# Performance work log

Hardware: AMD Instinct MI355X
Metric: run time of the kernel (lower is better)

Reference implementation:

```python
import jax, jax.numpy as jnp
import numpy as np

NW, OBS, HS, HS2, HM, CTX, ACT = 2048, 512, 512, 512, 256, 128, 18


def setup_inputs() -> dict:
    key = jax.random.key(0)
    ks = jax.random.split(key, 20)
    s = 0.02  # small init so tanh/softmax/sigmoid stay in sane range
    f32 = jnp.float32
    return {
        "obs": jax.random.normal(ks[0], (NW, 1, OBS), f32),
        "hidden_memory": jax.random.normal(ks[1], (1, NW, HM), f32),
        # fnn: Linear(obs_size, hidden_size)
        "W1": (jax.random.normal(ks[2], (HS, OBS), f32) * s),
        "b1": jnp.zeros((HS,), f32),
        # context: Linear(hidden_memory_size + 1, context_size)
        "Wc": (jax.random.normal(ks[3], (CTX, HM + 1), f32) * s),
        "bc": jnp.zeros((CTX,), f32),
        # attention: Linear(context_size, 1)
        "Wa": (jax.random.normal(ks[4], (1, CTX), f32) * s),
        "ba": jnp.zeros((1,), f32),
        # GRU(input=1, hidden=HM)
        "W_ih": (jax.random.normal(ks[5], (3 * HM, 1), f32) * s),
        "b_ih": jnp.zeros((3 * HM,), f32),
        "W_hh": (jax.random.normal(ks[6], (3 * HM, HM), f32) * s),
        "b_hh": jnp.zeros((3 * HM,), f32),
        # fnn2: Linear(hidden_size + hidden_memory_size, hidden_size_2)
        "W2": (jax.random.normal(ks[7], (HS2, HS + HM), f32) * s),
        "b2": jnp.zeros((HS2,), f32),
        # actor / critic heads
        "Wact": (jax.random.normal(ks[8], (ACT, HS2), f32) * s),
        "bact": jnp.zeros((ACT,), f32),
        "Wcrit": (jax.random.normal(ks[9], (1, HS2), f32) * s),
        "bcrit": jnp.zeros((1,), f32),
    }


def reference(obs, hidden_memory, W1, b1, Wc, bc, Wa, ba,
              W_ih, b_ih, W_hh, b_hh, W2, b2, Wact, bact, Wcrit, bcrit):
    # obs: [NW, 1, OBS], hidden_memory: [1, NW, HM]
    feat = jax.nn.relu(jnp.einsum('bto,ho->bth', obs, W1) + b1)  # [NW,1,HS]

    # context: Linear([obs_scalar, hidden_memory]) + tanh.
    # Split the (HM+1)-dim contraction: col 0 multiplies the obs scalar,
    # cols 1: contract with the broadcast hidden memory (same math as the
    # torch cat + Linear, without materializing the [NW,1,OBS,HM+1] tensor).
    h = jnp.swapaxes(hidden_memory, 0, 1)                        # [NW,1,HM]
    h_term = jnp.einsum('btm,cm->btc', h, Wc[:, 1:]) + bc        # [NW,1,CTX]
    ctx = jnp.tanh(obs[..., None] * Wc[:, 0] + h_term[:, :, None, :])  # [NW,1,OBS,CTX]

    # attention: Linear(CTX -> 1) then softmax over the obs dimension (dim=-2
    # of [...,OBS,1] == OBS after squeeze)
    alog = jnp.einsum('btoc,c->bto', ctx, Wa[0]) + ba[0]         # [NW,1,OBS]
    attn = jax.nn.softmax(alog, axis=-1)
    dset = jnp.sum(attn * obs, axis=-1, keepdims=True)           # [NW,1,1]

    # single-step GRU (torch gate ordering: r, z, n)
    x = dset[:, 0, :]                                            # [NW,1]
    hp = hidden_memory[0]                                        # [NW,HM]
    gi = x @ W_ih.T + b_ih                                       # [NW,3HM]
    gh = hp @ W_hh.T + b_hh
    ir, iz, inn = jnp.split(gi, 3, axis=-1)
    hr, hz, hn = jnp.split(gh, 3, axis=-1)
    r = jax.nn.sigmoid(ir + hr)
    z = jax.nn.sigmoid(iz + hz)
    n = jnp.tanh(inn + r * hn)
    hnew = (1.0 - z) * n + z * hp                                # [NW,HM]

    out = jnp.concatenate([feat[:, 0, :], hnew], axis=-1)        # [NW,HS+HM]
    out = jax.nn.relu(out @ W2.T + b2)                           # [NW,HS2]
    logits = out @ Wact.T + bact                                 # [NW,ACT]
    action = jax.random.categorical(jax.random.key(42), logits)  # [NW]
    log_prob = jax.nn.log_softmax(logits)[jnp.arange(logits.shape[0]), action]
    value = out @ Wcrit.T + bcrit                                # [NW,1]
    return (action, value, log_prob)
```

## Files before the change

### kernel.cpp

```cpp
#include <hip/hip_runtime.h>
#include <stdint.h>

#define NW   2048
#define OBS  512
#define HS   512
#define HS2  512
#define HM   256
#define CTX  128
#define ACT  18

#define K2LE 2.8853900817779268f

#define W1T_OFF   0
#define WCT_OFF   262144
#define W2T_OFF   294912
#define WHHQ_OFF  688128
#define FEAT_OFF  950272
#define GATES_OFF 1998848
#define HTERM_OFF 3571712
#define X_OFF     3833856
#define OUT2_OFF  3835904

#if __has_builtin(__builtin_amdgcn_exp2f)
#define EXP2F(x) __builtin_amdgcn_exp2f(x)
#else
#define EXP2F(x) exp2f(x)
#endif
#if __has_builtin(__builtin_amdgcn_rcpf)
#define RCPF(x) __builtin_amdgcn_rcpf(x)
#else
#define RCPF(x) (1.0f/(x))
#endif

#define TFR(x0, x1, R) { x0 += x1; x1 = (x1 << R) | (x1 >> (32 - R)); x1 ^= x0; }

__device__ __forceinline__ void threefry_0_42(uint32_t x0, uint32_t x1,
                                              uint32_t& o0, uint32_t& o1) {
    const uint32_t ks0 = 0u;
    const uint32_t ks1 = 42u;
    const uint32_t ks2 = 0x1BD11BDAu ^ ks0 ^ ks1;
    x0 += ks0; x1 += ks1;
    TFR(x0, x1, 13) TFR(x0, x1, 15) TFR(x0, x1, 26) TFR(x0, x1, 6)
    x0 += ks1; x1 += ks2 + 1u;
    TFR(x0, x1, 17) TFR(x0, x1, 29) TFR(x0, x1, 16) TFR(x0, x1, 24)
    x0 += ks2; x1 += ks0 + 2u;
    TFR(x0, x1, 13) TFR(x0, x1, 15) TFR(x0, x1, 26) TFR(x0, x1, 6)
    x0 += ks0; x1 += ks1 + 3u;
    TFR(x0, x1, 17) TFR(x0, x1, 29) TFR(x0, x1, 16) TFR(x0, x1, 24)
    x0 += ks1; x1 += ks2 + 4u;
    TFR(x0, x1, 13) TFR(x0, x1, 15) TFR(x0, x1, 26) TFR(x0, x1, 6)
    x0 += ks2; x1 += ks0 + 5u;
    o0 = x0; o1 = x1;
}

__device__ __forceinline__ float gumbel_ra(int row, int a) {
    uint32_t n = (uint32_t)(row * ACT + a);
    uint32_t o0, o1;
    threefry_0_42(0u, n, o0, o1);
    uint32_t bits = o0 ^ o1;
    uint32_t fb = (bits >> 9) | 0x3F800000u;
    float f = __uint_as_float(fb) - 1.0f;
    const float tiny = 1.17549435e-38f;
    float u = (f < tiny) ? tiny : f;
    return -logf(-logf(u));
}

__device__ __forceinline__ float fast_tanh(float x) {
    float e = __expf(2.0f * x);
    return 1.0f - 2.0f / (e + 1.0f);
}
__device__ __forceinline__ float fast_sig(float x) {
    return 1.0f / (1.0f + __expf(-x));
}

__global__ __launch_bounds__(256) void transpose_weights(
    const float* __restrict__ W1, const float* __restrict__ Wc,
    const float* __restrict__ Whh, const float* __restrict__ W2,
    float* __restrict__ ws)
{
    __shared__ float t[3][32][33];
    const int tx = threadIdx.x & 31, ty = threadIdx.x >> 5;
    int b = blockIdx.x;
    if (b < 672) {
        const float* src; float* dst; int ld, off, R, it, jt;
        if (b < 256)      { src = W1;  dst = ws + W1T_OFF;  ld = 512; off = 0; it = b >> 4; jt = b & 15; R = 512; }
        else if (b < 288) { int bb = b - 256; src = Wc;  dst = ws + WCT_OFF;  ld = 257; off = 1; it = bb >> 3; jt = bb & 7;  R = 128; }
        else              { int bb = b - 288; src = W2;  dst = ws + W2T_OFF;  ld = 768; off = 0; it = bb / 24; jt = bb % 24; R = 512; }
        const int i0 = it * 32, j0 = jt * 32;
        #pragma unroll
        for (int q = 0; q < 4; ++q)
            t[0][ty + 8 * q][tx] = src[(i0 + ty + 8 * q) * ld + off + j0 + tx];
        __syncthreads();
        #pragma unroll
        for (int q = 0; q < 4; ++q)
            dst[(j0 + ty + 8 * q) * R + i0 + tx] = t[0][tx][ty + 8 * q];
    } else {
        int bb = b - 672;
        const int mt = bb >> 3, jt = bb & 7;
        const int m0 = mt * 32, j0 = jt * 32;
        #pragma unroll
        for (int g = 0; g < 3; ++g)
            #pragma unroll
            for (int q = 0; q < 4; ++q)
                t[g][ty + 8 * q][tx] = Whh[(g * HM + j0 + ty + 8 * q) * HM + m0 + tx];
        __syncthreads();
        float4* dst = (float4*)(ws + WHHQ_OFF);
        #pragma unroll
        for (int q = 0; q < 4; ++q) {
            int ml = ty + 8 * q, jl = tx;
            dst[(size_t)(m0 + ml) * HM + j0 + jl] =
                make_float4(t[0][jl][ml], t[1][jl][ml], t[2][jl][ml], 0.0f);
        }
    }
}

__global__ __launch_bounds__(256) void gemm8(
    const float* __restrict__ obs, const float* __restrict__ hmem,
    const float* __restrict__ b1,  const float* __restrict__ bc,
    const float* __restrict__ bhh, float* __restrict__ ws)
{
    __shared__ float s_act[8 * 512];
    const int tid = threadIdx.x;
    const int wv = tid >> 6, lane = tid & 63;
    const int bid = blockIdx.x;

    if (bid < 256) {
        const int m0 = bid * 8;
        for (int i = tid; i < 1024; i += 256) {
            int r = i >> 7, kq = i & 127;
            *(float4*)&s_act[r * 512 + kq * 4] =
                *(const float4*)&obs[(size_t)(m0 + r) * 512 + kq * 4];
        }
        __syncthreads();
        const float2* __restrict__ Wt = (const float2*)(ws + W1T_OFF);
        const int c2 = wv * 64 + lane;
        float2 acc[8];
        #pragma unroll
        for (int r = 0; r < 8; ++r) acc[r] = make_float2(0.f, 0.f);
        #pragma unroll 4
        for (int k = 0; k < 512; k += 4) {
            float2 w0 = Wt[(k + 0) * 256 + c2];
            float2 w1 = Wt[(k + 1) * 256 + c2];
            float2 w2 = Wt[(k + 2) * 256 + c2];
            float2 w3 = Wt[(k + 3) * 256 + c2];
            #pragma unroll
            for (int r = 0; r < 8; ++r) {
                float4 o = *(const float4*)&s_act[r * 512 + k];
                acc[r].x = fmaf(o.x, w0.x, acc[r].x); acc[r].y = fmaf(o.x, w0.y, acc[r].y);
                acc[r].x = fmaf(o.y, w1.x, acc[r].x); acc[r].y = fmaf(o.y, w1.y, acc[r].y);
                acc[r].x = fmaf(o.z, w2.x, acc[r].x); acc[r].y = fmaf(o.z, w2.y, acc[r].y);
                acc[r].x = fmaf(o.w, w3.x, acc[r].x); acc[r].y = fmaf(o.w, w3.y, acc[r].y);
            }
        }
        float2 bb = ((const float2*)b1)[c2];
        float* F = ws + FEAT_OFF;
        #pragma unroll
        for (int r = 0; r < 8; ++r) {
            float2 v;
            v.x = fmaxf(acc[r].x + bb.x, 0.f);
            v.y = fmaxf(acc[r].y + bb.y, 0.f);
            *(float2*)&F[(size_t)(m0 + r) * 512 + c2 * 2] = v;
        }
    } else if (bid < 512) {
        const int m0 = (bid - 256) * 8;
        for (int i = tid; i < 512; i += 256) {
            int r = i >> 6, kq = i & 63;
            *(float4*)&s_act[r * 256 + kq * 4] =
                *(const float4*)&hmem[(size_t)(m0 + r) * 256 + kq * 4];
        }
        __syncthreads();
        const float4* __restrict__ Q = (const float4*)(ws + WHHQ_OFF);
        const int j = wv * 64 + lane;
        float ar[8] = {0,0,0,0,0,0,0,0}, az[8] = {0,0,0,0,0,0,0,0}, an[8] = {0,0,0,0,0,0,0,0};
        #pragma unroll 4
        for (int k = 0; k < 256; k += 4) {
            float4 q0 = Q[(k + 0) * 256 + j];
            float4 q1 = Q[(k + 1) * 256 + j];
            float4 q2 = Q[(k + 2) * 256 + j];
            float4 q3 = Q[(k + 3) * 256 + j];
            #pragma unroll
            for (int r = 0; r < 8; ++r) {
                float4 h = *(const float4*)&s_act[r * 256 + k];
                ar[r] = fmaf(h.x, q0.x, ar[r]); az[r] = fmaf(h.x, q0.y, az[r]); an[r] = fmaf(h.x, q0.z, an[r]);
                ar[r] = fmaf(h.y, q1.x, ar[r]); az[r] = fmaf(h.y, q1.y, az[r]); an[r] = fmaf(h.y, q1.z, an[r]);
                ar[r] = fmaf(h.z, q2.x, ar[r]); az[r] = fmaf(h.z, q2.y, az[r]); an[r] = fmaf(h.z, q2.z, an[r]);
                ar[r] = fmaf(h.w, q3.x, ar[r]); az[r] = fmaf(h.w, q3.y, az[r]); an[r] = fmaf(h.w, q3.z, an[r]);
            }
        }
        float br = bhh[j], bz = bhh[HM + j], bn = bhh[2 * HM + j];
        float* G = ws + GATES_OFF;
        #pragma unroll
        for (int r = 0; r < 8; ++r) {
            size_t base = (size_t)(m0 + r) * 768 + j;
            G[base]       = ar[r] + br;
            G[base + 256] = az[r] + bz;
            G[base + 512] = an[r] + bn;
        }
    } else {
        const int m0 = (bid - 512) * 8;
        for (int i = tid; i < 512; i += 256) {
            int r = i >> 6, kq = i & 63;
            *(float4*)&s_act[r * 256 + kq * 4] =
                *(const float4*)&hmem[(size_t)(m0 + r) * 256 + kq * 4];
        }
        __syncthreads();
        const float2* __restrict__ Wt = (const float2*)(ws + WCT_OFF);
        const int r0 = wv * 2;
        float2 a0 = make_float2(0.f, 0.f), a1 = make_float2(0.f, 0.f);
        #pragma unroll 4
        for (int k = 0; k < 256; k += 4) {
            float2 w0 = Wt[(k + 0) * 64 + lane];
            float2 w1 = Wt[(k + 1) * 64 + lane];
            float2 w2 = Wt[(k + 2) * 64 + lane];
            float2 w3 = Wt[(k + 3) * 64 + lane];
            float4 o0 = *(const float4*)&s_act[r0 * 256 + k];
            float4 o1 = *(const float4*)&s_act[(r0 + 1) * 256 + k];
            a0.x = fmaf(o0.x, w0.x, a0.x); a0.y = fmaf(o0.x, w0.y, a0.y);
            a0.x = fmaf(o0.y, w1.x, a0.x); a0.y = fmaf(o0.y, w1.y, a0.y);
            a0.x = fmaf(o0.z, w2.x, a0.x); a0.y = fmaf(o0.z, w2.y, a0.y);
            a0.x = fmaf(o0.w, w3.x, a0.x); a0.y = fmaf(o0.w, w3.y, a0.y);
            a1.x = fmaf(o1.x, w0.x, a1.x); a1.y = fmaf(o1.x, w0.y, a1.y);
            a1.x = fmaf(o1.y, w1.x, a1.x); a1.y = fmaf(o1.y, w1.y, a1.y);
            a1.x = fmaf(o1.z, w2.x, a1.x); a1.y = fmaf(o1.z, w2.y, a1.y);
            a1.x = fmaf(o1.w, w3.x, a1.x); a1.y = fmaf(o1.w, w3.y, a1.y);
        }
        float2 bb = ((const float2*)bc)[lane];
        float* H = ws + HTERM_OFF;
        float2 v0, v1;
        v0.x = K2LE * (a0.x + bb.x); v0.y = K2LE * (a0.y + bb.y);
        v1.x = K2LE * (a1.x + bb.x); v1.y = K2LE * (a1.y + bb.y);
        *(float2*)&H[(size_t)(m0 + r0) * 128 + lane * 2]     = v0;
        *(float2*)&H[(size_t)(m0 + r0 + 1) * 128 + lane * 2] = v1;
    }
}

__global__ __launch_bounds__(512) void attn_kernel(
    const float* __restrict__ obs, const float* __restrict__ Wc,
    const float* __restrict__ Wa,  const float* __restrict__ ba,
    float* __restrict__ ws)
{
    __shared__ float s_obs[4][512];
    __shared__ float s_ht[4][128];
    __shared__ float s_alog[4][512];
    __shared__ float s_wc0[128], s_wa2[128];

    const int tid = threadIdx.x;
    const int row0 = blockIdx.x * 4;
    const float* hterm = ws + HTERM_OFF;
    float* X = ws + X_OFF;

    {
        int r = tid >> 7, kq = tid & 127;
        *(float4*)&s_obs[r][kq * 4] =
            *(const float4*)&obs[(size_t)(row0 + r) * 512 + kq * 4];
    }
    if (tid < 128) {
        int r = tid >> 5, kq = tid & 31;
        *(float4*)&s_ht[r][kq * 4] =
            *(const float4*)&hterm[(size_t)(row0 + r) * 128 + kq * 4];
    } else if (tid < 256) {
        int t = tid - 128;
        s_wc0[t] = K2LE * Wc[t * (HM + 1)];
        s_wa2[t] = 2.0f * Wa[t];
    }
    __syncthreads();

    {
        const float ba0 = ba[0];
        const int o = tid;
        float ob[4], acA[4];
        #pragma unroll
        for (int r = 0; r < 4; ++r) { ob[r] = s_obs[r][o]; acA[r] = 0.f; }
        float swa = 0.f;
        for (int c = 0; c < 128; c += 4) {
            float4 v = *(const float4*)&s_wa2[c];
            swa += v.x + v.y + v.z + v.w;
        }
        swa *= 0.5f;
        for (int c4 = 0; c4 < 32; ++c4) {
            float4 wc = *(const float4*)&s_wc0[c4 * 4];
            float4 wa = *(const float4*)&s_wa2[c4 * 4];
            #pragma unroll
            for (int r = 0; r < 4; ++r) {
                float4 ht = *(const float4*)&s_ht[r][c4 * 4];
                float t0 = fmaf(ob[r], wc.x, ht.x);
                acA[r] = fmaf(wa.x, RCPF(EXP2F(t0) + 1.f), acA[r]);
                float t1 = fmaf(ob[r], wc.y, ht.y);
                acA[r] = fmaf(wa.y, RCPF(EXP2F(t1) + 1.f), acA[r]);
                float t2 = fmaf(ob[r], wc.z, ht.z);
                acA[r] = fmaf(wa.z, RCPF(EXP2F(t2) + 1.f), acA[r]);
                float t3 = fmaf(ob[r], wc.w, ht.w);
                acA[r] = fmaf(wa.w, RCPF(EXP2F(t3) + 1.f), acA[r]);
            }
        }
        #pragma unroll
        for (int r = 0; r < 4; ++r) s_alog[r][o] = ba0 + swa - acA[r];
    }
    __syncthreads();

    {
        const int wv = tid >> 6, lane = tid & 63;
        if (wv < 4) {
            const int r = wv;
            float m = -1e30f;
            for (int o = lane; o < 512; o += 64) m = fmaxf(m, s_alog[r][o]);
            #pragma unroll
            for (int d = 32; d >= 1; d >>= 1) m = fmaxf(m, __shfl_xor(m, d));
            float se = 0.f, sw = 0.f;
            for (int o = lane; o < 512; o += 64) {
                float e = __expf(s_alog[r][o] - m);
                se += e; sw += e * s_obs[r][o];
            }
            #pragma unroll
            for (int d = 32; d >= 1; d >>= 1) { se += __shfl_xor(se, d); sw += __shfl_xor(sw, d); }
            if (lane == 0) X[row0 + r] = sw / se;
        }
    }
}

__global__ __launch_bounds__(512) void out2_gemm(
    const float* __restrict__ hmem,  const float* __restrict__ W_ih,
    const float* __restrict__ b_ih,  const float* __restrict__ b2,
    const float* __restrict__ ws_c,  float* __restrict__ ws)
{
    __shared__ float s_act[8 * 768];
    __shared__ float s_P[6144];
    const int tid = threadIdx.x;
    const int wv = tid >> 6, lane = tid & 63;
    const int rowb = blockIdx.x >> 1, colb = blockIdx.x & 1;
    const int m0 = rowb * 8;
    const float* F = ws_c + FEAT_OFF;
    const float* G = ws_c + GATES_OFF;
    const float* X = ws_c + X_OFF;

    for (int i = tid; i < 1024; i += 512) {
        int r = i >> 7, kq = i & 127;
        *(float4*)&s_act[r * 768 + kq * 4] =
            *(const float4*)&F[(size_t)(m0 + r) * 512 + kq * 4];
    }
    for (int i = tid; i < 2048; i += 512) {
        int r = i >> 8, j = i & 255;
        int grow = m0 + r;
        float g0 = G[(size_t)grow * 768 + j];
        float g1 = G[(size_t)grow * 768 + 256 + j];
        float g2 = G[(size_t)grow * 768 + 512 + j];
        float hp = hmem[(size_t)grow * 256 + j];
        float x  = X[grow];
        float rg = fast_sig(fmaf(x, W_ih[j], b_ih[j]) + g0);
        float zg = fast_sig(fmaf(x, W_ih[256 + j], b_ih[256 + j]) + g1);
        float ng = fast_tanh(fmaf(x, W_ih[512 + j], b_ih[512 + j]) + rg * g2);
        s_act[r * 768 + 512 + j] = (1.0f - zg) * ng + zg * hp;
    }
    __syncthreads();

    const float2* __restrict__ Wt = (const float2*)(ws_c + W2T_OFF);
    const int kg = wv & 3, cg = wv >> 2;
    const int c2 = colb * 128 + cg * 64 + lane;
    const int k0 = kg * 192;
    float2 acc[8];
    #pragma unroll
    for (int r = 0; r < 8; ++r) acc[r] = make_float2(0.f, 0.f);
    #pragma unroll 4
    for (int k = k0; k < k0 + 192; k += 4) {
        float2 w0 = Wt[(k + 0) * 256 + c2];
        float2 w1 = Wt[(k + 1) * 256 + c2];
        float2 w2 = Wt[(k + 2) * 256 + c2];
        float2 w3 = Wt[(k + 3) * 256 + c2];
        #pragma unroll
        for (int r = 0; r < 8; ++r) {
            float4 o = *(const float4*)&s_act[r * 768 + k];
            acc[r].x = fmaf(o.x, w0.x, acc[r].x); acc[r].y = fmaf(o.x, w0.y, acc[r].y);
            acc[r].x = fmaf(o.y, w1.x, acc[r].x); acc[r].y = fmaf(o.y, w1.y, acc[r].y);
            acc[r].x = fmaf(o.z, w2.x, acc[r].x); acc[r].y = fmaf(o.z, w2.y, acc[r].y);
            acc[r].x = fmaf(o.w, w3.x, acc[r].x); acc[r].y = fmaf(o.w, w3.y, acc[r].y);
        }
    }
    float2* P2 = (float2*)s_P;
    const int cl = cg * 64 + lane;
    if (kg != 0) {
        #pragma unroll
        for (int r = 0; r < 8; ++r) P2[((kg - 1) * 8 + r) * 128 + cl] = acc[r];
    }
    __syncthreads();
    if (kg == 0) {
        float2 bb = ((const float2*)b2)[c2];
        float* O = ws + OUT2_OFF;
        #pragma unroll
        for (int r = 0; r < 8; ++r) {
            float2 p0 = P2[(0 * 8 + r) * 128 + cl];
            float2 p1 = P2[(1 * 8 + r) * 128 + cl];
            float2 p2 = P2[(2 * 8 + r) * 128 + cl];
            float2 v;
            v.x = fmaxf(acc[r].x + p0.x + p1.x + p2.x + bb.x, 0.f);
            v.y = fmaxf(acc[r].y + p0.y + p1.y + p2.y + bb.y, 0.f);
            *(float2*)&ws[OUT2_OFF + (size_t)(m0 + r) * 512 + c2 * 2] = v;
        }
        (void)O;
    }
}

__global__ __launch_bounds__(512) void heads_kernel(
    const float* __restrict__ Wact,  const float* __restrict__ bact,
    const float* __restrict__ Wcrit, const float* __restrict__ bcrit,
    const float* __restrict__ ws,    float* __restrict__ out)
{
    const int wv = threadIdx.x >> 6, lane = threadIdx.x & 63;
    const int grow = blockIdx.x * 8 + wv;
    const float* o2 = ws + OUT2_OFF;

    float4 x0 = *(const float4*)&o2[(size_t)grow * 512 + lane * 8];
    float4 x1 = *(const float4*)&o2[(size_t)grow * 512 + lane * 8 + 4];

    float la[ACT];
    #pragma unroll
    for (int a = 0; a < ACT; ++a) {
        const float4* wa4 = (const float4*)&Wact[a * HS2 + lane * 8];
        float4 w0 = wa4[0], w1 = wa4[1];
        float p = x0.x * w0.x + x0.y * w0.y + x0.z * w0.z + x0.w * w0.w
                + x1.x * w1.x + x1.y * w1.y + x1.z * w1.z + x1.w * w1.w;
        #pragma unroll
        for (int d = 32; d >= 1; d >>= 1) p += __shfl_xor(p, d);
        la[a] = p + bact[a];
    }
    const float4* wc4 = (const float4*)&Wcrit[lane * 8];
    float4 w0 = wc4[0], w1 = wc4[1];
    float pv = x0.x * w0.x + x0.y * w0.y + x0.z * w0.z + x0.w * w0.w
             + x1.x * w1.x + x1.y * w1.y + x1.z * w1.z + x1.w * w1.w;
    #pragma unroll
    for (int d = 32; d >= 1; d >>= 1) pv += __shfl_xor(pv, d);

    float g = (lane < ACT) ? gumbel_ra(grow, lane) : 0.0f;
    float best = -1e30f; int amax = 0;
    float mx = -1e30f;
    #pragma unroll
    for (int a = 0; a < ACT; ++a) {
        float g_ = __shfl(g, a);
        float y = la[a] + g_;
        if (y > best) { best = y; amax = a; }
        mx = fmaxf(mx, la[a]);
    }
    float se = 0.f;
    #pragma unroll
    for (int a = 0; a < ACT; ++a) se += __expf(la[a] - mx);
    float lse = mx + logf(se);
    float lp = la[amax] - lse;
    if (lane == 0) {
        out[grow]          = (float)amax;
        out[NW + grow]     = pv + bcrit[0];
        out[2 * NW + grow] = lp;
    }
}

extern "C" void kernel_launch(void* const* d_in, const int* in_sizes, int n_in,
                              void* d_out, int out_size, void* d_ws, size_t ws_size,
                              hipStream_t stream) {
    const float* obs   = (const float*)d_in[0];
    const float* hmem  = (const float*)d_in[1];
    const float* W1    = (const float*)d_in[2];
    const float* b1    = (const float*)d_in[3];
    const float* Wc    = (const float*)d_in[4];
    const float* bc    = (const float*)d_in[5];
    const float* Wa    = (const float*)d_in[6];
    const float* ba    = (const float*)d_in[7];
    const float* W_ih  = (const float*)d_in[8];
    const float* b_ih  = (const float*)d_in[9];
    const float* W_hh  = (const float*)d_in[10];
    const float* b_hh  = (const float*)d_in[11];
    const float* W2    = (const float*)d_in[12];
    const float* b2    = (const float*)d_in[13];
    const float* Wact  = (const float*)d_in[14];
    const float* bact  = (const float*)d_in[15];
    const float* Wcrit = (const float*)d_in[16];
    const float* bcrit = (const float*)d_in[17];
    float* ws = (float*)d_ws;

    transpose_weights<<<736, 256, 0, stream>>>(W1, Wc, W_hh, W2, ws);
    gemm8<<<768, 256, 0, stream>>>(obs, hmem, b1, bc, b_hh, ws);
    attn_kernel<<<512, 512, 0, stream>>>(obs, Wc, Wa, ba, ws);
    out2_gemm<<<512, 512, 0, stream>>>(hmem, W_ih, b_ih, b2, ws, ws);
    heads_kernel<<<256, 512, 0, stream>>>(Wact, bact, Wcrit, bcrit, ws, (float*)d_out);
}
```

Measured before the change: 119.2 us.

## Retile FFN, GRU and context GEMMs to 16-row blocks with scalar columns

The gemm kernel now processes 16 activation rows per block instead of 8. Each thread computes one scalar column instead of a float2 pair, and the W1 block is split into two column halves. out2_gemm likewise uses 16 rows with 4 column blocks and reuses the activation shared buffer for the split-K partials instead of a separate s_P array. The aim is to halve weight reads from global or L2 per output row and reduce grid size, at the cost of higher register pressure (48 GRU accumulators) and more shared memory per block, which may lower occupancy.

```diff
diff --git a/kernel.cpp b/kernel.cpp
--- a/kernel.cpp
+++ b/kernel.cpp
@@ -114,72 +114,69 @@
     }
 }
 
-__global__ __launch_bounds__(256) void gemm8(
+__global__ __launch_bounds__(256) void gemm16(
     const float* __restrict__ obs, const float* __restrict__ hmem,
     const float* __restrict__ b1,  const float* __restrict__ bc,
     const float* __restrict__ bhh, float* __restrict__ ws)
 {
-    __shared__ float s_act[8 * 512];
+    __shared__ float s_act[16 * 512];
     const int tid = threadIdx.x;
-    const int wv = tid >> 6, lane = tid & 63;
     const int bid = blockIdx.x;
 
     if (bid < 256) {
-        const int m0 = bid * 8;
-        for (int i = tid; i < 1024; i += 256) {
+        const int m0 = (bid >> 1) * 16;
+        const int c  = (bid & 1) * 256 + tid;
+        for (int i = tid; i < 2048; i += 256) {
             int r = i >> 7, kq = i & 127;
             *(float4*)&s_act[r * 512 + kq * 4] =
                 *(const float4*)&obs[(size_t)(m0 + r) * 512 + kq * 4];
         }
         __syncthreads();
-        const float2* __restrict__ Wt = (const float2*)(ws + W1T_OFF);
-        const int c2 = wv * 64 + lane;
-        float2 acc[8];
-        #pragma unroll
-        for (int r = 0; r < 8; ++r) acc[r] = make_float2(0.f, 0.f);
+        const float* __restrict__ Wt = ws + W1T_OFF;
+        float acc[16];
+        #pragma unroll
+        for (int r = 0; r < 16; ++r) acc[r] = 0.f;
         #pragma unroll 4
-        for (int k = 0; k < 512; k += 4) {
-            float2 w0 = Wt[(k + 0) * 256 + c2];
-            float2 w1 = Wt[(k + 1) * 256 + c2];
-            float2 w2 = Wt[(k + 2) * 256 + c2];
-            float2 w3 = Wt[(k + 3) * 256 + c2];
-            #pragma unroll
-            for (int r = 0; r < 8; ++r) {
+        for (int k4 = 0; k4 < 128; ++k4) {
+            const int k = k4 * 4;
+            float w0 = Wt[(k + 0) * 512 + c];
+            float w1 = Wt[(k + 1) * 512 + c];
+            float w2 = Wt[(k + 2) * 512 + c];
+            float w3 = Wt[(k + 3) * 512 + c];
+            #pragma unroll
+            for (int r = 0; r < 16; ++r) {
                 float4 o = *(const float4*)&s_act[r * 512 + k];
-                acc[r].x = fmaf(o.x, w0.x, acc[r].x); acc[r].y = fmaf(o.x, w0.y, acc[r].y);
-                acc[r].x = fmaf(o.y, w1.x, acc[r].x); acc[r].y = fmaf(o.y, w1.y, acc[r].y);
-                acc[r].x = fmaf(o.z, w2.x, acc[r].x); acc[r].y = fmaf(o.z, w2.y, acc[r].y);
-                acc[r].x = fmaf(o.w, w3.x, acc[r].x); acc[r].y = fmaf(o.w, w3.y, acc[r].y);
+                acc[r] = fmaf(o.x, w0, acc[r]); acc[r] = fmaf(o.y, w1, acc[r]);
+                acc[r] = fmaf(o.z, w2, acc[r]); acc[r] = fmaf(o.w, w3, acc[r]);
             }
         }
-        float2 bb = ((const float2*)b1)[c2];
+        float bb = b1[c];
         float* F = ws + FEAT_OFF;
         #pragma unroll
-        for (int r = 0; r < 8; ++r) {
-            float2 v;
-            v.x = fmaxf(acc[r].x + bb.x, 0.f);
-            v.y = fmaxf(acc[r].y + bb.y, 0.f);
-            *(float2*)&F[(size_t)(m0 + r) * 512 + c2 * 2] = v;
-        }
-    } else if (bid < 512) {
-        const int m0 = (bid - 256) * 8;
-        for (int i = tid; i < 512; i += 256) {
+        for (int r = 0; r < 16; ++r)
+            F[(size_t)(m0 + r) * 512 + c] = fmaxf(acc[r] + bb, 0.f);
+    } else if (bid < 384) {
+        const int m0 = (bid - 256) * 16;
+        for (int i = tid; i < 1024; i += 256) {
             int r = i >> 6, kq = i & 63;
             *(float4*)&s_act[r * 256 + kq * 4] =
                 *(const float4*)&hmem[(size_t)(m0 + r) * 256 + kq * 4];
         }
         __syncthreads();
         const float4* __restrict__ Q = (const float4*)(ws + WHHQ_OFF);
-        const int j = wv * 64 + lane;
-        float ar[8] = {0,0,0,0,0,0,0,0}, az[8] = {0,0,0,0,0,0,0,0}, an[8] = {0,0,0,0,0,0,0,0};
-        #pragma unroll 4
-        for (int k = 0; k < 256; k += 4) {
+        const int j = tid;
+        float ar[16], az[16], an[16];
+        #pragma unroll
+        for (int r = 0; r < 16; ++r) { ar[r] = 0.f; az[r] = 0.f; an[r] = 0.f; }
+        #pragma unroll 2
+        for (int k4 = 0; k4 < 64; ++k4) {
+            const int k = k4 * 4;
             float4 q0 = Q[(k + 0) * 256 + j];
             float4 q1 = Q[(k + 1) * 256 + j];
             float4 q2 = Q[(k + 2) * 256 + j];
             float4 q3 = Q[(k + 3) * 256 + j];
             #pragma unroll
-            for (int r = 0; r < 8; ++r) {
+            for (int r = 0; r < 16; ++r) {
                 float4 h = *(const float4*)&s_act[r * 256 + k];
                 ar[r] = fmaf(h.x, q0.x, ar[r]); az[r] = fmaf(h.x, q0.y, az[r]); an[r] = fmaf(h.x, q0.z, an[r]);
                 ar[r] = fmaf(h.y, q1.x, ar[r]); az[r] = fmaf(h.y, q1.y, az[r]); an[r] = fmaf(h.y, q1.z, an[r]);
@@ -190,47 +187,45 @@
         float br = bhh[j], bz = bhh[HM + j], bn = bhh[2 * HM + j];
         float* G = ws + GATES_OFF;
         #pragma unroll
-        for (int r = 0; r < 8; ++r) {
+        for (int r = 0; r < 16; ++r) {
             size_t base = (size_t)(m0 + r) * 768 + j;
             G[base]       = ar[r] + br;
             G[base + 256] = az[r] + bz;
             G[base + 512] = an[r] + bn;
         }
     } else {
-        const int m0 = (bid - 512) * 8;
-        for (int i = tid; i < 512; i += 256) {
+        const int m0 = (bid - 384) * 16;
+        for (int i = tid; i < 1024; i += 256) {
             int r = i >> 6, kq = i & 63;
             *(float4*)&s_act[r * 256 + kq * 4] =
                 *(const float4*)&hmem[(size_t)(m0 + r) * 256 + kq * 4];
         }
         __syncthreads();
-        const float2* __restrict__ Wt = (const float2*)(ws + WCT_OFF);
-        const int r0 = wv * 2;
-        float2 a0 = make_float2(0.f, 0.f), a1 = make_float2(0.f, 0.f);
+        const float* __restrict__ Wt = ws + WCT_OFF;
+        const int c  = tid & 127;
+        const int r0 = (tid >> 7) * 8;
+        float acc[8];
+        #pragma unroll
+        for (int r = 0; r < 8; ++r) acc[r] = 0.f;
         #pragma unroll 4
-        for (int k = 0; k < 256; k += 4) {
-            float2 w0 = Wt[(k + 0) * 64 + lane];
-            float2 w1 = Wt[(k + 1) * 64 + lane];
-            float2 w2 = Wt[(k + 2) * 64 + lane];
-            float2 w3 = Wt[(k + 3) * 64 + lane];
-            float4 o0 = *(const float4*)&s_act[r0 * 256 + k];
-            float4 o1 = *(const float4*)&s_act[(r0 + 1) * 256 + k];
-            a0.x = fmaf(o0.x, w0.x, a0.x); a0.y = fmaf(o0.x, w0.y, a0.y);
-            a0.x = fmaf(o0.y, w1.x, a0.x); a0.y = fmaf(o0.y, w1.y, a0.y);
-            a0.x = fmaf(o0.z, w2.x, a0.x); a0.y = fmaf(o0.z, w2.y, a0.y);
-            a0.x = fmaf(o0.w, w3.x, a0.x); a0.y = fmaf(o0.w, w3.y, a0.y);
-            a1.x = fmaf(o1.x, w0.x, a1.x); a1.y = fmaf(o1.x, w0.y, a1.y);
-            a1.x = fmaf(o1.y, w1.x, a1.x); a1.y = fmaf(o1.y, w1.y, a1.y);
-            a1.x = fmaf(o1.z, w2.x, a1.x); a1.y = fmaf(o1.z, w2.y, a1.y);
-            a1.x = fmaf(o1.w, w3.x, a1.x); a1.y = fmaf(o1.w, w3.y, a1.y);
-        }
-        float2 bb = ((const float2*)bc)[lane];
+        for (int k4 = 0; k4 < 64; ++k4) {
+            const int k = k4 * 4;
+            float w0 = Wt[(k + 0) * 128 + c];
+            float w1 = Wt[(k + 1) * 128 + c];
+            float w2 = Wt[(k + 2) * 128 + c];
+            float w3 = Wt[(k + 3) * 128 + c];
+            #pragma unroll
+            for (int r = 0; r < 8; ++r) {
+                float4 h = *(const float4*)&s_act[(r0 + r) * 256 + k];
+                acc[r] = fmaf(h.x, w0, acc[r]); acc[r] = fmaf(h.y, w1, acc[r]);
+                acc[r] = fmaf(h.z, w2, acc[r]); acc[r] = fmaf(h.w, w3, acc[r]);
+            }
+        }
+        float bb = bc[c];
         float* H = ws + HTERM_OFF;
-        float2 v0, v1;
-        v0.x = K2LE * (a0.x + bb.x); v0.y = K2LE * (a0.y + bb.y);
-        v1.x = K2LE * (a1.x + bb.x); v1.y = K2LE * (a1.y + bb.y);
-        *(float2*)&H[(size_t)(m0 + r0) * 128 + lane * 2]     = v0;
-        *(float2*)&H[(size_t)(m0 + r0 + 1) * 128 + lane * 2] = v1;
+        #pragma unroll
+        for (int r = 0; r < 8; ++r)
+            H[(size_t)(m0 + r0 + r) * 128 + c] = K2LE * (acc[r] + bb);
     }
 }
 
@@ -321,24 +316,23 @@
 __global__ __launch_bounds__(512) void out2_gemm(
     const float* __restrict__ hmem,  const float* __restrict__ W_ih,
     const float* __restrict__ b_ih,  const float* __restrict__ b2,
-    const float* __restrict__ ws_c,  float* __restrict__ ws)
+    float* __restrict__ ws)
 {
-    __shared__ float s_act[8 * 768];
-    __shared__ float s_P[6144];
+    __shared__ float s_act[16 * 768];
     const int tid = threadIdx.x;
     const int wv = tid >> 6, lane = tid & 63;
-    const int rowb = blockIdx.x >> 1, colb = blockIdx.x & 1;
-    const int m0 = rowb * 8;
-    const float* F = ws_c + FEAT_OFF;
-    const float* G = ws_c + GATES_OFF;
-    const float* X = ws_c + X_OFF;
-
-    for (int i = tid; i < 1024; i += 512) {
+    const int rowb = blockIdx.x >> 2, colb = blockIdx.x & 3;
+    const int m0 = rowb * 16;
+    const float* F = ws + FEAT_OFF;
+    const float* G = ws + GATES_OFF;
+    const float* X = ws + X_OFF;
+
+    for (int i = tid; i < 2048; i += 512) {
         int r = i >> 7, kq = i & 127;
         *(float4*)&s_act[r * 768 + kq * 4] =
             *(const float4*)&F[(size_t)(m0 + r) * 512 + kq * 4];
     }
-    for (int i = tid; i < 2048; i += 512) {
+    for (int i = tid; i < 4096; i += 512) {
         int r = i >> 8, j = i & 255;
         int grow = m0 + r;
         float g0 = G[(size_t)grow * 768 + j];
@@ -353,49 +347,45 @@
     }
     __syncthreads();
 
-    const float2* __restrict__ Wt = (const float2*)(ws_c + W2T_OFF);
+    const float* __restrict__ Wt = ws + W2T_OFF;
     const int kg = wv & 3, cg = wv >> 2;
-    const int c2 = colb * 128 + cg * 64 + lane;
+    const int cl = cg * 64 + lane;
+    const int c  = colb * 128 + cl;
     const int k0 = kg * 192;
-    float2 acc[8];
+    float acc[16];
     #pragma unroll
-    for (int r = 0; r < 8; ++r) acc[r] = make_float2(0.f, 0.f);
+    for (int r = 0; r < 16; ++r) acc[r] = 0.f;
     #pragma unroll 4
-    for (int k = k0; k < k0 + 192; k += 4) {
-        float2 w0 = Wt[(k + 0) * 256 + c2];
-        float2 w1 = Wt[(k + 1) * 256 + c2];
-        float2 w2 = Wt[(k + 2) * 256 + c2];
-        float2 w3 = Wt[(k + 3) * 256 + c2];
-        #pragma unroll
-        for (int r = 0; r < 8; ++r) {
+    for (int k4 = 0; k4 < 48; ++k4) {
+        const int k = k0 + k4 * 4;
+        float w0 = Wt[(k + 0) * 512 + c];
+        float w1 = Wt[(k + 1) * 512 + c];
+        float w2 = Wt[(k + 2) * 512 + c];
+        float w3 = Wt[(k + 3) * 512 + c];
+        #pragma unroll
+        for (int r = 0; r < 16; ++r) {
             float4 o = *(const float4*)&s_act[r * 768 + k];
-            acc[r].x = fmaf(o.x, w0.x, acc[r].x); acc[r].y = fmaf(o.x, w0.y, acc[r].y);
-            acc[r].x = fmaf(o.y, w1.x, acc[r].x); acc[r].y = fmaf(o.y, w1.y, acc[r].y);
-            acc[r].x = fmaf(o.z, w2.x, acc[r].x); acc[r].y = fmaf(o.z, w2.y, acc[r].y);
-            acc[r].x = fmaf(o.w, w3.x, acc[r].x); acc[r].y = fmaf(o.w, w3.y, acc[r].y);
-        }
-    }
-    float2* P2 = (float2*)s_P;
-    const int cl = cg * 64 + lane;
+            acc[r] = fmaf(o.x, w0, acc[r]); acc[r] = fmaf(o.y, w1, acc[r]);
+            acc[r] = fmaf(o.z, w2, acc[r]); acc[r] = fmaf(o.w, w3, acc[r]);
+        }
+    }
+    __syncthreads();
+    float* P = s_act;
     if (kg != 0) {
         #pragma unroll
-        for (int r = 0; r < 8; ++r) P2[((kg - 1) * 8 + r) * 128 + cl] = acc[r];
+        for (int r = 0; r < 16; ++r) P[((kg - 1) * 16 + r) * 128 + cl] = acc[r];
     }
     __syncthreads();
     if (kg == 0) {
-        float2 bb = ((const float2*)b2)[c2];
+        float bb = b2[c];
         float* O = ws + OUT2_OFF;
         #pragma unroll
-        for (int r = 0; r < 8; ++r) {
-            float2 p0 = P2[(0 * 8 + r) * 128 + cl];
-            float2 p1 = P2[(1 * 8 + r) * 128 + cl];
-            float2 p2 = P2[(2 * 8 + r) * 128 + cl];
-            float2 v;
-            v.x = fmaxf(acc[r].x + p0.x + p1.x + p2.x + bb.x, 0.f);
-            v.y = fmaxf(acc[r].y + p0.y + p1.y + p2.y + bb.y, 0.f);
-            *(float2*)&ws[OUT2_OFF + (size_t)(m0 + r) * 512 + c2 * 2] = v;
-        }
-        (void)O;
+        for (int r = 0; r < 16; ++r) {
+            float v = acc[r] + P[(0 * 16 + r) * 128 + cl]
+                             + P[(1 * 16 + r) * 128 + cl]
+                             + P[(2 * 16 + r) * 128 + cl] + bb;
+            O[(size_t)(m0 + r) * 512 + c] = fmaxf(v, 0.f);
+        }
     }
 }
 
@@ -475,8 +465,8 @@
     float* ws = (float*)d_ws;
 
     transpose_weights<<<736, 256, 0, stream>>>(W1, Wc, W_hh, W2, ws);
-    gemm8<<<768, 256, 0, stream>>>(obs, hmem, b1, bc, b_hh, ws);
+    gemm16<<<512, 256, 0, stream>>>(obs, hmem, b1, bc, b_hh, ws);
     attn_kernel<<<512, 512, 0, stream>>>(obs, Wc, Wa, ba, ws);
-    out2_gemm<<<512, 512, 0, stream>>>(hmem, W_ih, b_ih, b2, ws, ws);
+    out2_gemm<<<512, 512, 0, stream>>>(hmem, W_ih, b_ih, b2, ws);
     heads_kernel<<<256, 512, 0, stream>>>(Wact, bact, Wcrit, bcrit, ws, (float*)d_out);
 }
```

Result: slower. 174.7 us (+46.6%).
